# Kernel tuning notes

Hardware: AMD Instinct MI355X
Metric: run time of the kernel (lower is better)

The kernel has to match this reference:

```python
import jax, jax.numpy as jnp
import numpy as np

EPS = 1e-20
TEMP = 0.07
HEAD_DIM = 128


def setup_inputs() -> dict:
    key = jax.random.key(0)
    k1, k2, k3 = jax.random.split(key, 3)
    B, C, T, H, W = 4, 512, 8, 32, 32
    x = jax.random.normal(k1, (B, C, T, H, W), dtype=jnp.float32)
    W_head = jax.random.normal(k2, (C, HEAD_DIM), dtype=jnp.float32) / np.sqrt(C).astype(np.float32)
    b_head = jax.random.normal(k3, (HEAD_DIM,), dtype=jnp.float32) * 0.01
    return {"x": x, "W_head": W_head, "b_head": b_head}


def _forward(x, W_head, b_head):
    B, C, T, H, W = x.shape
    N = H * W
    # linear head over channel dim (equivalent to permute->Linear->permute)
    feats = jnp.einsum('bcthw,cd->bdthw', x, W_head) + b_head[None, :, None, None, None]
    keys = feats.reshape(B, HEAD_DIM, T, N)
    # F.normalize(p=2, dim=1): x / max(||x||, 1e-12)
    norm = jnp.maximum(jnp.linalg.norm(keys, axis=1, keepdims=True), 1e-12)
    keys = keys / norm
    # affinity between consecutive frames: [B, T-1, N, N]
    A = jnp.einsum('bctn,bctm->btnm', keys[:, :, :-1], keys[:, :, 1:])
    A12 = jax.nn.softmax(A / TEMP, axis=-1)                         # forward stochastic mats
    A21 = jax.nn.softmax(jnp.swapaxes(A, -1, -2) / TEMP, axis=-1)   # backward stochastic mats
    A12s = jnp.swapaxes(A12, 0, 1)  # [T-1, B, N, N]
    A21s = jnp.swapaxes(A21, 0, 1)  # [T-1, B, N, N]

    # prefix products P[i] = A12[0] @ A12[1] @ ... @ A12[i]
    def step_p(carry, a):
        c = carry @ a
        return c, c
    _, Ptail = jax.lax.scan(step_p, A12s[0], A12s[1:])
    P = jnp.concatenate([A12s[:1], Ptail], axis=0)  # [T-1, B, N, N]

    # suffix products S[i] = A21[i] @ A21[i-1] @ ... @ A21[0]
    def step_s(carry, a):
        c = a @ carry
        return c, c
    _, Stail = jax.lax.scan(step_s, A21s[0], A21s[1:])
    S = jnp.concatenate([A21s[:1], Stail], axis=0)  # [T-1, B, N, N]

    # cycle walks for i = 1..T-2: aar_i = P[i] @ S[i]
    aars = jnp.matmul(P[1:], S[1:])  # [T-2, B, N, N]
    logits = jnp.log(aars + EPS)
    # cross-entropy with identity targets: loss = logsumexp - logit[n, n]
    lse = jax.nn.logsumexp(logits, axis=-1)                  # [T-2, B, N]
    diag = jnp.diagonal(logits, axis1=-2, axis2=-1)          # [T-2, B, N]
    losses = jnp.mean(lse - diag, axis=(1, 2))               # [T-2]
    preds = jnp.argmax(logits, axis=-1)                      # [T-2, B, N]
    tgt = jnp.arange(N)[None, None, :]
    accs = jnp.mean((preds == tgt).astype(jnp.float32), axis=(1, 2))
    # original returns (loss_of_last_walk, diags); diags exposed as stacked arrays
    return losses[-1], losses, accs


def reference(x, W_head, b_head):
    return _forward(x, W_head, b_head)
```

## Files before the change

### kernel.cpp

```cpp
#include <hip/hip_runtime.h>
#include <cstdint>
#include <cstddef>

typedef unsigned short u16;
typedef unsigned long long u64;
using short8 = __attribute__((ext_vector_type(8))) short;
using f32x4  = __attribute__((ext_vector_type(4))) float;

#define KEXP 20.609929155556620f

__device__ __forceinline__ u16 f2bf(float f) {
  unsigned u = __float_as_uint(f);
  u += 0x7fffu + ((u >> 16) & 1u);
  return (u16)(u >> 16);
}
__device__ __forceinline__ float bf2f(u16 h) { return __uint_as_float(((unsigned)h) << 16); }

typedef const unsigned int GASu32 __attribute__((address_space(1)));
typedef unsigned int LASu32 __attribute__((address_space(3)));

__device__ __forceinline__ void gload16(const u16* src, u16* dstLds) {
  __builtin_amdgcn_global_load_lds((GASu32*)src, (LASu32*)dstLds, 16, 0, 0);
}

__global__ __launch_bounds__(256) void transpose_x(const float* __restrict__ x, u16* __restrict__ xT) {
  __shared__ float t[32][33];
  int b = blockIdx.z, c0 = blockIdx.y * 32, s0 = blockIdx.x * 32;
  int tid = threadIdx.x;
  int ci = tid >> 3, s4 = (tid & 7) * 4;
  float4 v = *(const float4*)(x + ((size_t)b * 512 + c0 + ci) * 8192 + s0 + s4);
  t[ci][s4 + 0] = v.x; t[ci][s4 + 1] = v.y; t[ci][s4 + 2] = v.z; t[ci][s4 + 3] = v.w;
  __syncthreads();
  int si = tid >> 3, c4 = (tid & 7) * 4;
  ushort4 o;
  o.x = f2bf(t[c4 + 0][si]); o.y = f2bf(t[c4 + 1][si]);
  o.z = f2bf(t[c4 + 2][si]); o.w = f2bf(t[c4 + 3][si]);
  *(ushort4*)(xT + ((size_t)b * 8192 + s0 + si) * 512 + c0 + c4) = o;
}

__global__ __launch_bounds__(256) void transpose_w(const float* __restrict__ W, u16* __restrict__ Wt) {
  int idx = blockIdx.x * 256 + threadIdx.x;
  int d = idx >> 9, c = idx & 511;
  Wt[idx] = f2bf(W[c * 128 + d]);
}

__global__ __launch_bounds__(256) void normalize_keys(u16* __restrict__ keys) {
  int wv = threadIdx.x >> 6, lane = threadIdx.x & 63;
  int row = blockIdx.x * 4 + wv;
  unsigned* p = (unsigned*)(keys + (size_t)row * 128) + lane;
  unsigned v = *p;
  float a = bf2f((u16)(v & 0xffffu)), b = bf2f((u16)(v >> 16));
  float s = a * a + b * b;
  #pragma unroll
  for (int m = 1; m < 64; m <<= 1) s += __shfl_xor(s, m, 64);
  float sc = 1.f / fmaxf(sqrtf(s), 1e-12f);
  *p = (unsigned)f2bf(a * sc) | ((unsigned)f2bf(b * sc) << 16);
}

__global__ __launch_bounds__(256) void k3_t0(const u16* __restrict__ E, const float* __restrict__ rsum,
                                             const float* __restrict__ csum,
                                             u16* __restrict__ P0, u16* __restrict__ S0) {
  int b = blockIdx.z, r = blockIdx.x;
  int zE = b * 7;
  const u16* e = E + ((size_t)zE << 20) + (size_t)r * 1024;
  float rr = 1.f / rsum[zE * 1024 + r];
  int c = threadIdx.x * 4;
  ushort4 v = *(const ushort4*)(e + c);
  float4 cv = *(const float4*)(csum + zE * 1024 + c);
  ushort4 o1, o2;
  float v0 = bf2f(v.x), v1 = bf2f(v.y), v2 = bf2f(v.z), v3 = bf2f(v.w);
  o1.x = f2bf(v0 * rr); o1.y = f2bf(v1 * rr); o1.z = f2bf(v2 * rr); o1.w = f2bf(v3 * rr);
  o2.x = f2bf(v0 / cv.x); o2.y = f2bf(v1 / cv.y); o2.z = f2bf(v2 / cv.z); o2.w = f2bf(v3 / cv.w);
  size_t base = ((size_t)b << 20) + (size_t)r * 1024 + c;
  *(ushort4*)(P0 + base) = o1;
  *(ushort4*)(S0 + base) = o2;
}

__global__ __launch_bounds__(256) void k3_tr(const u16* __restrict__ E, const float* __restrict__ rsum,
                                             const float* __restrict__ csum,
                                             u16* __restrict__ Bp, u16* __restrict__ Bs) {
  __shared__ u16 t[64][66];
  int z = blockIdx.z; int b = z / 6, tt = z % 6 + 1;
  int zE = b * 7 + tt;
  int er0 = blockIdx.x * 64, ec0 = blockIdx.y * 64;
  const u16* e = E + ((size_t)zE << 20);
  int tid = threadIdx.x;
  int ri = tid >> 4, c4 = (tid & 15) * 4;
  #pragma unroll
  for (int p = 0; p < 4; ++p) {
    ushort4 v = *(const ushort4*)(e + (size_t)(er0 + ri + p * 16) * 1024 + ec0 + c4);
    t[ri + p * 16][c4 + 0] = v.x; t[ri + p * 16][c4 + 1] = v.y;
    t[ri + p * 16][c4 + 2] = v.z; t[ri + p * 16][c4 + 3] = v.w;
  }
  __syncthreads();
  size_t outBase = (size_t)(b * 6 + tt - 1) << 20;
  float ir0 = 1.f / rsum[zE * 1024 + er0 + c4 + 0];
  float ir1 = 1.f / rsum[zE * 1024 + er0 + c4 + 1];
  float ir2 = 1.f / rsum[zE * 1024 + er0 + c4 + 2];
  float ir3 = 1.f / rsum[zE * 1024 + er0 + c4 + 3];
  #pragma unroll
  for (int p = 0; p < 4; ++p) {
    int roL = ri + p * 16;
    int ro = ec0 + roL;
    float ic = 1.f / csum[zE * 1024 + ro];
    float v0 = bf2f(t[c4 + 0][roL]), v1 = bf2f(t[c4 + 1][roL]);
    float v2 = bf2f(t[c4 + 2][roL]), v3 = bf2f(t[c4 + 3][roL]);
    ushort4 op, os;
    op.x = f2bf(v0 * ir0); op.y = f2bf(v1 * ir1); op.z = f2bf(v2 * ir2); op.w = f2bf(v3 * ir3);
    os.x = f2bf(v0 * ic);  os.y = f2bf(v1 * ic);  os.z = f2bf(v2 * ic);  os.w = f2bf(v3 * ic);
    size_t off = outBase + (size_t)ro * 1024 + er0 + c4;
    *(ushort4*)(Bp + off) = op;
    *(ushort4*)(Bs + off) = os;
  }
}

struct GemmBatch { const u16* A[24]; const u16* B[24]; u16* C[8]; };
enum { M_HEAD = 0, M_EXP = 1, M_PLAIN = 2, M_AAR = 3 };

__device__ __forceinline__ int lds_off32(int r, int kbyte) {
  int rp = r >> 1;
  int sl = (((r & 1) << 2) | (kbyte >> 4)) ^ (rp & 7);
  return rp * 128 + sl * 16;
}

__device__ __forceinline__ void stage_tile32(const u16* __restrict__ g, int ld, int r0, int k0, u16* lds) {
  int tid = threadIdx.x;
  #pragma unroll
  for (int j = 0; j < 2; ++j) {
    int gidx = j * 256 + tid;
    int rp = gidx >> 3, slot = gidx & 7;
    int sp = slot ^ (rp & 7);
    int r = (rp << 1) | (sp >> 2);
    int kb16 = sp & 3;
    const u16* src = g + (size_t)(r0 + r) * ld + k0 + kb16 * 8;
    gload16(src, lds + gidx * 8);
  }
}

__device__ __forceinline__ short8 frag_ld32(const u16* s, int row, int kbyte) {
  return *(const short8*)((const char*)s + lds_off32(row, kbyte));
}

#define GEMM_BODY(T, FA, FB, NA, NB)                                                    \
  {                                                                                     \
    int t_ = (T);                                                                       \
    if (t_ + 1 < nt) {                                                                  \
      if (t_ + 2 < nt) asm volatile("s_waitcnt vmcnt(4)" ::: "memory");                 \
      else             asm volatile("s_waitcnt vmcnt(0)" ::: "memory");                 \
      __builtin_amdgcn_s_barrier();                                                     \
      __builtin_amdgcn_sched_barrier(0);                                                \
      const u16* An_ = As[(t_ + 1) & 3];                                                \
      const u16* Bn_ = Bs[(t_ + 1) & 3];                                                \
      _Pragma("unroll")                                                                 \
      for (int f = 0; f < 4; ++f) {                                                     \
        NA[f] = frag_ld32(An_, (wr << 6) + (f << 4) + l15, kb);                         \
        NB[f] = frag_ld32(Bn_, (wc << 6) + (f << 4) + l15, kb);                         \
      }                                                                                 \
      if (t_ + 3 < nt) {                                                                \
        stage_tile32(A, lda, m0, (t_ + 3) << 5, As[(t_ + 3) & 3]);                      \
        stage_tile32(B, ldb, n0, (t_ + 3) << 5, Bs[(t_ + 3) & 3]);                      \
      }                                                                                 \
      asm volatile("s_waitcnt lgkmcnt(8)" ::: "memory");                                \
    } else {                                                                            \
      asm volatile("s_waitcnt lgkmcnt(0)" ::: "memory");                                \
    }                                                                                   \
    __builtin_amdgcn_sched_barrier(0);                                                  \
    __builtin_amdgcn_s_setprio(1);                                                      \
    _Pragma("unroll")                                                                   \
    for (int fr = 0; fr < 4; ++fr)                                                      \
      _Pragma("unroll")                                                                 \
      for (int fc2 = 0; fc2 < 4; ++fc2)                                                 \
        acc[fr][fc2] = __builtin_amdgcn_mfma_f32_16x16x32_bf16(FA[fr], FB[fc2],         \
                                                               acc[fr][fc2], 0, 0, 0); \
    __builtin_amdgcn_s_setprio(0);                                                      \
  }

template <int MODE>
__global__ __launch_bounds__(256) void gemm_nt(const u16* __restrict__ gA, const u16* __restrict__ gB,
                                               u16* __restrict__ gC, GemmBatch batch,
                                               const float* __restrict__ bias,
                                               float* __restrict__ rowsumR, u64* __restrict__ amax,
                                               float* __restrict__ diagv,
                                               float* __restrict__ rsumE, float* __restrict__ csumE) {
  __shared__ u16 As[4][4096];
  __shared__ u16 Bs[4][4096];
  int tid = threadIdx.x, lane = tid & 63, wv = tid >> 6;
  int wr = wv >> 1, wc = wv & 1;
  int l15 = lane & 15, kb = (lane >> 4) << 4;

  int swz;
  { int per = (int)gridDim.x >> 3; int id0 = blockIdx.x; swz = (id0 & 7) * per + (id0 >> 3); }
  int z, m0, n0;
  if constexpr (MODE == M_HEAD) { z = 0; m0 = swz << 7; n0 = 0; }
  else { z = swz >> 6; int r6 = swz & 63; m0 = (r6 & 7) << 7; n0 = (r6 >> 3) << 7; }

  const u16 *A, *B; u16* C;
  int K, lda, ldb, ldc;
  if constexpr (MODE == M_HEAD) {
    A = gA; B = gB; C = gC; K = 512; lda = 512; ldb = 512; ldc = 128;
  } else if constexpr (MODE == M_EXP) {
    int b = z / 7, t = z % 7;
    size_t offA = (size_t)(b * 8 + t) * 131072;
    A = gA + offA; B = gA + offA + 131072; C = gC + ((size_t)z << 20);
    K = 128; lda = 128; ldb = 128; ldc = 1024;
  } else if constexpr (MODE == M_PLAIN) {
    A = batch.A[z]; B = batch.B[z]; C = batch.C[z];
    K = 1024; lda = 1024; ldb = 1024; ldc = 1024;
  } else {
    A = batch.A[z]; B = batch.B[z]; C = nullptr;
    K = 1024; lda = 1024; ldb = 1024; ldc = 1024;
  }

  f32x4 acc[4][4] = {};
  int nt = K >> 5;

  stage_tile32(A, lda, m0, 0,  As[0]); stage_tile32(B, ldb, n0, 0,  Bs[0]);
  stage_tile32(A, lda, m0, 32, As[1]); stage_tile32(B, ldb, n0, 32, Bs[1]);
  stage_tile32(A, lda, m0, 64, As[2]); stage_tile32(B, ldb, n0, 64, Bs[2]);
  asm volatile("s_waitcnt vmcnt(8)" ::: "memory");
  __builtin_amdgcn_s_barrier();
  __builtin_amdgcn_sched_barrier(0);
  short8 fa0[4], fb0[4], fa1[4], fb1[4];
  #pragma unroll
  for (int f = 0; f < 4; ++f) {
    fa0[f] = frag_ld32(As[0], (wr << 6) + (f << 4) + l15, kb);
    fb0[f] = frag_ld32(Bs[0], (wc << 6) + (f << 4) + l15, kb);
  }

  for (int t = 0; t < nt; t += 2) {
    GEMM_BODY(t,     fa0, fb0, fa1, fb1);
    GEMM_BODY(t + 1, fa1, fb1, fa0, fb0);
  }

  if constexpr (MODE == M_AAR) {
    #pragma unroll
    for (int fr = 0; fr < 4; ++fr) {
      #pragma unroll
      for (int j = 0; j < 4; ++j) {
        float rs = 0.f, mv = -1.f; int mc = 0;
        #pragma unroll
        for (int fc = 0; fc < 4; ++fc) {
          float v = acc[fr][fc][j];
          rs += v;
          int c = n0 + (wc << 6) + (fc << 4) + l15;
          if (v > mv) { mv = v; mc = c; }
        }
        u64 pk = ((u64)__float_as_uint(mv) << 32) | (u64)(unsigned)(1023 - mc);
        #pragma unroll
        for (int m = 1; m < 16; m <<= 1) {
          rs += __shfl_xor(rs, m, 64);
          u64 o = __shfl_xor(pk, m, 64);
          pk = (o > pk) ? o : pk;
        }
        if (l15 == 0) {
          int row = m0 + (wr << 6) + (fr << 4) + ((lane >> 4) << 2) + j;
          atomicAdd(&rowsumR[(z << 10) + row], rs);
          atomicMax(&amax[(z << 10) + row], pk);
        }
      }
      if (m0 == n0 && wr == wc) {
        int jj = l15 - ((lane >> 4) << 2);
        if (jj >= 0 && jj < 4) {
          int row = m0 + (wr << 6) + (fr << 4) + l15;
          float dv = (jj == 0) ? acc[fr][fr][0] : (jj == 1) ? acc[fr][fr][1]
                    : (jj == 2) ? acc[fr][fr][2] : acc[fr][fr][3];
          diagv[(z << 10) + row] = dv;
        }
      }
    }
  } else if constexpr (MODE == M_EXP) {
    float rp[4][4] = {};
    float cp[4] = {};
    #pragma unroll
    for (int fr = 0; fr < 4; ++fr)
      #pragma unroll
      for (int fc = 0; fc < 4; ++fc)
        #pragma unroll
        for (int j = 0; j < 4; ++j) {
          int row = m0 + (wr << 6) + (fr << 4) + ((lane >> 4) << 2) + j;
          int col = n0 + (wc << 6) + (fc << 4) + l15;
          float v = exp2f(acc[fr][fc][j] * KEXP);
          C[(size_t)row * ldc + col] = f2bf(v);
          rp[fr][j] += v;
          cp[fc] += v;
        }
    #pragma unroll
    for (int fr = 0; fr < 4; ++fr)
      #pragma unroll
      for (int j = 0; j < 4; ++j) {
        float r = rp[fr][j];
        r += __shfl_xor(r, 1, 64); r += __shfl_xor(r, 2, 64);
        r += __shfl_xor(r, 4, 64); r += __shfl_xor(r, 8, 64);
        if (l15 == 0) {
          int row = m0 + (wr << 6) + (fr << 4) + ((lane >> 4) << 2) + j;
          atomicAdd(&rsumE[z * 1024 + row], r);
        }
      }
    #pragma unroll
    for (int fc = 0; fc < 4; ++fc) {
      float c = cp[fc];
      c += __shfl_xor(c, 16, 64); c += __shfl_xor(c, 32, 64);
      if ((lane >> 4) == 0) {
        int col = n0 + (wc << 6) + (fc << 4) + l15;
        atomicAdd(&csumE[z * 1024 + col], c);
      }
    }
  } else {
    #pragma unroll
    for (int fr = 0; fr < 4; ++fr)
      #pragma unroll
      for (int fc = 0; fc < 4; ++fc)
        #pragma unroll
        for (int j = 0; j < 4; ++j) {
          int row = m0 + (wr << 6) + (fr << 4) + ((lane >> 4) << 2) + j;
          int col = n0 + (wc << 6) + (fc << 4) + l15;
          float v = acc[fr][fc][j];
          if constexpr (MODE == M_HEAD) v += bias[col];
          C[(size_t)row * ldc + col] = f2bf(v);
        }
  }
}

__global__ __launch_bounds__(256) void finalize_k(const float* __restrict__ rowsumR, const u64* __restrict__ amax,
                                                  const float* __restrict__ diagv, float* __restrict__ out) {
  __shared__ float sl[256], sa[256];
  int w = blockIdx.x;
  int tid = threadIdx.x;
  float ls = 0.f, ac = 0.f;
  for (int idx = tid; idx < 4096; idx += 256) {
    int zi = (w << 12) + idx;
    int n = idx & 1023;
    float rs = rowsumR[zi];
    float dv = diagv[zi];
    ls += logf(rs + 1024.f * 1e-20f) - logf(dv + 1e-20f);
    unsigned pred = 1023u - (unsigned)(amax[zi] & 0xffffffffULL);
    ac += (pred == (unsigned)n) ? 1.f : 0.f;
  }
  sl[tid] = ls; sa[tid] = ac;
  __syncthreads();
  for (int s2 = 128; s2 > 0; s2 >>= 1) {
    if (tid < s2) { sl[tid] += sl[tid + s2]; sa[tid] += sa[tid + s2]; }
    __syncthreads();
  }
  if (tid == 0) {
    float loss = sl[0] / 4096.f, acv = sa[0] / 4096.f;
    out[1 + w] = loss;
    out[7 + w] = acv;
    if (w == 5) out[0] = loss;
  }
}

extern "C" void kernel_launch(void* const* d_in, const int* in_sizes, int n_in,
                              void* d_out, int out_size, void* d_ws, size_t ws_size,
                              hipStream_t stream) {
  (void)in_sizes; (void)n_in; (void)out_size; (void)ws_size;
  const float* x  = (const float*)d_in[0];
  const float* Wh = (const float*)d_in[1];
  const float* bh = (const float*)d_in[2];
  float* out = (float*)d_out;
  char* ws = (char*)d_ws;
  const size_t MB = 1ull << 20;

  u16* xT   = (u16*)(ws);
  u16* keys = (u16*)(ws + 32 * MB);
  u16* Wt   = (u16*)(ws + 40 * MB);
  float* rsumE   = (float*)(ws + 40 * MB + 128 * 1024);
  float* csumE   = (float*)(ws + 40 * MB + 240 * 1024);
  float* rowsumR = (float*)(ws + 40 * MB + 352 * 1024);
  u64*   amax    = (u64*)(ws + 40 * MB + 448 * 1024);
  float* diagv   = (float*)(ws + 40 * MB + 640 * 1024);
  u16* E    = (u16*)(ws + 41 * MB);
  u16* Bp   = (u16*)(ws + 113 * MB);
  u16* Bs   = (u16*)(ws + 161 * MB);

  u16* Pb[7] = { (u16*)(ws + 97 * MB), (u16*)(ws + 0 * MB), (u16*)(ws + 8 * MB),
                 (u16*)(ws + 16 * MB), (u16*)(ws + 24 * MB), (u16*)(ws + 41 * MB),
                 (u16*)(ws + 49 * MB) };
  u16* Sb[7] = { (u16*)(ws + 105 * MB), (u16*)(ws + 57 * MB), (u16*)(ws + 65 * MB),
                 (u16*)(ws + 73 * MB), (u16*)(ws + 81 * MB), (u16*)(ws + 89 * MB),
                 (u16*)(ws + 97 * MB) };

  GemmBatch empty{};

  transpose_x<<<dim3(256, 16, 4), 256, 0, stream>>>(x, xT);
  transpose_w<<<dim3(256), 256, 0, stream>>>(Wh, Wt);
  gemm_nt<M_HEAD><<<dim3(256), 256, 0, stream>>>(xT, Wt, keys, empty, bh,
                                                 nullptr, nullptr, nullptr, nullptr, nullptr);
  normalize_keys<<<dim3(8192), 256, 0, stream>>>(keys);
  (void)hipMemsetAsync(rsumE, 0, 512 * 1024, stream);
  gemm_nt<M_EXP><<<dim3(1792), 256, 0, stream>>>(keys, nullptr, E, empty, nullptr,
                                                 nullptr, nullptr, nullptr, rsumE, csumE);
  k3_t0<<<dim3(1024, 1, 4), 256, 0, stream>>>(E, rsumE, csumE, Pb[0], Sb[0]);
  k3_tr<<<dim3(16, 16, 24), 256, 0, stream>>>(E, rsumE, csumE, Bp, Bs);

  for (int i = 1; i <= 6; ++i) {
    GemmBatch gb{};
    for (int b = 0; b < 4; ++b) {
      gb.A[b]     = Pb[i - 1] + (size_t)b * 1048576;
      gb.B[b]     = Bp + (size_t)(b * 6 + i - 1) * 1048576;
      gb.C[b]     = Pb[i] + (size_t)b * 1048576;
      gb.A[4 + b] = Sb[i - 1] + (size_t)b * 1048576;
      gb.B[4 + b] = Bs + (size_t)(b * 6 + i - 1) * 1048576;
      gb.C[4 + b] = Sb[i] + (size_t)b * 1048576;
    }
    gemm_nt<M_PLAIN><<<dim3(512), 256, 0, stream>>>(nullptr, nullptr, nullptr, gb, nullptr,
                                                    nullptr, nullptr, nullptr, nullptr, nullptr);
  }

  GemmBatch ga{};
  for (int i = 1; i <= 6; ++i)
    for (int b = 0; b < 4; ++b) {
      ga.A[(i - 1) * 4 + b] = Pb[i] + (size_t)b * 1048576;
      ga.B[(i - 1) * 4 + b] = Sb[i] + (size_t)b * 1048576;
    }
  gemm_nt<M_AAR><<<dim3(1536), 256, 0, stream>>>(nullptr, nullptr, nullptr, ga, nullptr,
                                                 rowsumR, amax, diagv, nullptr, nullptr);
  finalize_k<<<dim3(6), 256, 0, stream>>>(rowsumR, amax, diagv, out);
}
```

Measured before the change: 314.7 us.

## Shrink GEMM LDS ring to three stages with precomputed load addresses

The GEMM pipeline's LDS ring goes from four stages to three, with rotating buffer pointers instead of modulo indexing. Per-thread global source pointers and LDS fragment offsets are now computed once before the loop rather than every iteration. Prefetch depth drops from three tiles ahead to two, and each step waits for all outstanding global loads (vmcnt(0)). This cuts address arithmetic and LDS footprint, which may allow higher occupancy, but gives less latency hiding for global loads.

```diff
diff --git a/kernel.cpp b/kernel.cpp
--- a/kernel.cpp
+++ b/kernel.cpp
@@ -123,42 +123,24 @@
   return rp * 128 + sl * 16;
 }
 
-__device__ __forceinline__ void stage_tile32(const u16* __restrict__ g, int ld, int r0, int k0, u16* lds) {
-  int tid = threadIdx.x;
-  #pragma unroll
-  for (int j = 0; j < 2; ++j) {
-    int gidx = j * 256 + tid;
-    int rp = gidx >> 3, slot = gidx & 7;
-    int sp = slot ^ (rp & 7);
-    int r = (rp << 1) | (sp >> 2);
-    int kb16 = sp & 3;
-    const u16* src = g + (size_t)(r0 + r) * ld + k0 + kb16 * 8;
-    gload16(src, lds + gidx * 8);
-  }
-}
-
-__device__ __forceinline__ short8 frag_ld32(const u16* s, int row, int kbyte) {
-  return *(const short8*)((const char*)s + lds_off32(row, kbyte));
-}
-
 #define GEMM_BODY(T, FA, FB, NA, NB)                                                    \
   {                                                                                     \
     int t_ = (T);                                                                       \
     if (t_ + 1 < nt) {                                                                  \
-      if (t_ + 2 < nt) asm volatile("s_waitcnt vmcnt(4)" ::: "memory");                 \
-      else             asm volatile("s_waitcnt vmcnt(0)" ::: "memory");                 \
+      asm volatile("s_waitcnt vmcnt(0)" ::: "memory");                                  \
       __builtin_amdgcn_s_barrier();                                                     \
       __builtin_amdgcn_sched_barrier(0);                                                \
-      const u16* An_ = As[(t_ + 1) & 3];                                                \
-      const u16* Bn_ = Bs[(t_ + 1) & 3];                                                \
       _Pragma("unroll")                                                                 \
       for (int f = 0; f < 4; ++f) {                                                     \
-        NA[f] = frag_ld32(An_, (wr << 6) + (f << 4) + l15, kb);                         \
-        NB[f] = frag_ld32(Bn_, (wc << 6) + (f << 4) + l15, kb);                         \
+        NA[f] = *(const short8*)((const char*)An + offA[f]);                            \
+        NB[f] = *(const short8*)((const char*)Bn + offB[f]);                            \
       }                                                                                 \
-      if (t_ + 3 < nt) {                                                                \
-        stage_tile32(A, lda, m0, (t_ + 3) << 5, As[(t_ + 3) & 3]);                      \
-        stage_tile32(B, ldb, n0, (t_ + 3) << 5, Bs[(t_ + 3) & 3]);                      \
+      if (t_ + 2 < nt) {                                                                \
+        int k0_ = (t_ + 2) << 5;                                                        \
+        gload16(srcA0 + k0_, At + ldso0);                                               \
+        gload16(srcA1 + k0_, At + ldso1);                                               \
+        gload16(srcB0 + k0_, Bt + ldso0);                                               \
+        gload16(srcB1 + k0_, Bt + ldso1);                                               \
       }                                                                                 \
       asm volatile("s_waitcnt lgkmcnt(8)" ::: "memory");                                \
     } else {                                                                            \
@@ -173,6 +155,8 @@
         acc[fr][fc2] = __builtin_amdgcn_mfma_f32_16x16x32_bf16(FA[fr], FB[fc2],         \
                                                                acc[fr][fc2], 0, 0, 0); \
     __builtin_amdgcn_s_setprio(0);                                                      \
+    { u16* tmpA = Ac; Ac = An; An = At; At = tmpA;                                      \
+      u16* tmpB = Bc; Bc = Bn; Bn = Bt; Bt = tmpB; }                                    \
   }
 
 template <int MODE>
@@ -182,8 +166,8 @@
                                                float* __restrict__ rowsumR, u64* __restrict__ amax,
                                                float* __restrict__ diagv,
                                                float* __restrict__ rsumE, float* __restrict__ csumE) {
-  __shared__ u16 As[4][4096];
-  __shared__ u16 Bs[4][4096];
+  __shared__ u16 AsL[3][4096];
+  __shared__ u16 BsL[3][4096];
   int tid = threadIdx.x, lane = tid & 63, wv = tid >> 6;
   int wr = wv >> 1, wc = wv & 1;
   int l15 = lane & 15, kb = (lane >> 4) << 4;
@@ -200,8 +184,8 @@
     A = gA; B = gB; C = gC; K = 512; lda = 512; ldb = 512; ldc = 128;
   } else if constexpr (MODE == M_EXP) {
     int b = z / 7, t = z % 7;
-    size_t offA = (size_t)(b * 8 + t) * 131072;
-    A = gA + offA; B = gA + offA + 131072; C = gC + ((size_t)z << 20);
+    size_t offA0 = (size_t)(b * 8 + t) * 131072;
+    A = gA + offA0; B = gA + offA0 + 131072; C = gC + ((size_t)z << 20);
     K = 128; lda = 128; ldb = 128; ldc = 1024;
   } else if constexpr (MODE == M_PLAIN) {
     A = batch.A[z]; B = batch.B[z]; C = batch.C[z];
@@ -211,20 +195,45 @@
     K = 1024; lda = 1024; ldb = 1024; ldc = 1024;
   }
 
+  const u16 *srcA0, *srcA1, *srcB0, *srcB1;
+  int ldso0, ldso1;
+  {
+    int g0 = tid, g1 = 256 + tid;
+    int rp0 = g0 >> 3, sp0 = (g0 & 7) ^ (rp0 & 7);
+    int r0_ = (rp0 << 1) | (sp0 >> 2), kb0 = (sp0 & 3) * 8;
+    int rp1 = g1 >> 3, sp1 = (g1 & 7) ^ (rp1 & 7);
+    int r1_ = (rp1 << 1) | (sp1 >> 2), kb1 = (sp1 & 3) * 8;
+    srcA0 = A + (size_t)(m0 + r0_) * lda + kb0;
+    srcA1 = A + (size_t)(m0 + r1_) * lda + kb1;
+    srcB0 = B + (size_t)(n0 + r0_) * ldb + kb0;
+    srcB1 = B + (size_t)(n0 + r1_) * ldb + kb1;
+    ldso0 = g0 * 8; ldso1 = g1 * 8;
+  }
+  int offA[4], offB[4];
+  #pragma unroll
+  for (int f = 0; f < 4; ++f) {
+    offA[f] = lds_off32((wr << 6) + (f << 4) + l15, kb);
+    offB[f] = lds_off32((wc << 6) + (f << 4) + l15, kb);
+  }
+
   f32x4 acc[4][4] = {};
   int nt = K >> 5;
 
-  stage_tile32(A, lda, m0, 0,  As[0]); stage_tile32(B, ldb, n0, 0,  Bs[0]);
-  stage_tile32(A, lda, m0, 32, As[1]); stage_tile32(B, ldb, n0, 32, Bs[1]);
-  stage_tile32(A, lda, m0, 64, As[2]); stage_tile32(B, ldb, n0, 64, Bs[2]);
-  asm volatile("s_waitcnt vmcnt(8)" ::: "memory");
+  u16 *Ac = AsL[0], *An = AsL[1], *At = AsL[2];
+  u16 *Bc = BsL[0], *Bn = BsL[1], *Bt = BsL[2];
+
+  gload16(srcA0 +  0, Ac + ldso0); gload16(srcA1 +  0, Ac + ldso1);
+  gload16(srcB0 +  0, Bc + ldso0); gload16(srcB1 +  0, Bc + ldso1);
+  gload16(srcA0 + 32, An + ldso0); gload16(srcA1 + 32, An + ldso1);
+  gload16(srcB0 + 32, Bn + ldso0); gload16(srcB1 + 32, Bn + ldso1);
+  asm volatile("s_waitcnt vmcnt(4)" ::: "memory");
   __builtin_amdgcn_s_barrier();
   __builtin_amdgcn_sched_barrier(0);
   short8 fa0[4], fb0[4], fa1[4], fb1[4];
   #pragma unroll
   for (int f = 0; f < 4; ++f) {
-    fa0[f] = frag_ld32(As[0], (wr << 6) + (f << 4) + l15, kb);
-    fb0[f] = frag_ld32(Bs[0], (wc << 6) + (f << 4) + l15, kb);
+    fa0[f] = *(const short8*)((const char*)Ac + offA[f]);
+    fb0[f] = *(const short8*)((const char*)Bc + offB[f]);
   }
 
   for (int t = 0; t < nt; t += 2) {
```

New measurement: 324.9 us. 1.03x slower.

## Fuse cycle-walk AAR GEMMs into chain GEMM launches and drop atomics

Applied to the files above, without the earlier changes.

The separate batched AAR GEMM launch is removed. Each walk's P[i]@S[i] GEMM now runs inside the same launch as the next chain step, so the chain launches, which only fill 512 blocks, get extra independent blocks. Per-row sums and argmax are written as per-column-block partials instead of global atomics, and the finalize kernel reduces the 16 partials. This removes a memset, the atomic traffic and one large launch. In exchange it adds extra partial-buffer traffic, and the chain kernel carries a branchy epilogue.

```diff
diff --git a/kernel.cpp b/kernel.cpp
--- a/kernel.cpp
+++ b/kernel.cpp
@@ -115,7 +115,7 @@
 }
 
 struct GemmBatch { const u16* A[24]; const u16* B[24]; u16* C[8]; };
-enum { M_HEAD = 0, M_EXP = 1, M_PLAIN = 2, M_AAR = 3 };
+enum { M_HEAD = 0, M_EXP = 1 };
 
 __device__ __forceinline__ int lds_off32(int r, int kbyte) {
   int rp = r >> 1;
@@ -177,10 +177,8 @@
 
 template <int MODE>
 __global__ __launch_bounds__(256) void gemm_nt(const u16* __restrict__ gA, const u16* __restrict__ gB,
-                                               u16* __restrict__ gC, GemmBatch batch,
+                                               u16* __restrict__ gC,
                                                const float* __restrict__ bias,
-                                               float* __restrict__ rowsumR, u64* __restrict__ amax,
-                                               float* __restrict__ diagv,
                                                float* __restrict__ rsumE, float* __restrict__ csumE) {
   __shared__ u16 As[4][4096];
   __shared__ u16 Bs[4][4096];
@@ -198,17 +196,11 @@
   int K, lda, ldb, ldc;
   if constexpr (MODE == M_HEAD) {
     A = gA; B = gB; C = gC; K = 512; lda = 512; ldb = 512; ldc = 128;
-  } else if constexpr (MODE == M_EXP) {
+  } else {
     int b = z / 7, t = z % 7;
-    size_t offA = (size_t)(b * 8 + t) * 131072;
-    A = gA + offA; B = gA + offA + 131072; C = gC + ((size_t)z << 20);
+    size_t offA0 = (size_t)(b * 8 + t) * 131072;
+    A = gA + offA0; B = gA + offA0 + 131072; C = gC + ((size_t)z << 20);
     K = 128; lda = 128; ldb = 128; ldc = 1024;
-  } else if constexpr (MODE == M_PLAIN) {
-    A = batch.A[z]; B = batch.B[z]; C = batch.C[z];
-    K = 1024; lda = 1024; ldb = 1024; ldc = 1024;
-  } else {
-    A = batch.A[z]; B = batch.B[z]; C = nullptr;
-    K = 1024; lda = 1024; ldb = 1024; ldc = 1024;
   }
 
   f32x4 acc[4][4] = {};
@@ -226,49 +218,12 @@
     fa0[f] = frag_ld32(As[0], (wr << 6) + (f << 4) + l15, kb);
     fb0[f] = frag_ld32(Bs[0], (wc << 6) + (f << 4) + l15, kb);
   }
-
   for (int t = 0; t < nt; t += 2) {
     GEMM_BODY(t,     fa0, fb0, fa1, fb1);
     GEMM_BODY(t + 1, fa1, fb1, fa0, fb0);
   }
 
-  if constexpr (MODE == M_AAR) {
-    #pragma unroll
-    for (int fr = 0; fr < 4; ++fr) {
-      #pragma unroll
-      for (int j = 0; j < 4; ++j) {
-        float rs = 0.f, mv = -1.f; int mc = 0;
-        #pragma unroll
-        for (int fc = 0; fc < 4; ++fc) {
-          float v = acc[fr][fc][j];
-          rs += v;
-          int c = n0 + (wc << 6) + (fc << 4) + l15;
-          if (v > mv) { mv = v; mc = c; }
-        }
-        u64 pk = ((u64)__float_as_uint(mv) << 32) | (u64)(unsigned)(1023 - mc);
-        #pragma unroll
-        for (int m = 1; m < 16; m <<= 1) {
-          rs += __shfl_xor(rs, m, 64);
-          u64 o = __shfl_xor(pk, m, 64);
-          pk = (o > pk) ? o : pk;
-        }
-        if (l15 == 0) {
-          int row = m0 + (wr << 6) + (fr << 4) + ((lane >> 4) << 2) + j;
-          atomicAdd(&rowsumR[(z << 10) + row], rs);
-          atomicMax(&amax[(z << 10) + row], pk);
-        }
-      }
-      if (m0 == n0 && wr == wc) {
-        int jj = l15 - ((lane >> 4) << 2);
-        if (jj >= 0 && jj < 4) {
-          int row = m0 + (wr << 6) + (fr << 4) + l15;
-          float dv = (jj == 0) ? acc[fr][fr][0] : (jj == 1) ? acc[fr][fr][1]
-                    : (jj == 2) ? acc[fr][fr][2] : acc[fr][fr][3];
-          diagv[(z << 10) + row] = dv;
-        }
-      }
-    }
-  } else if constexpr (MODE == M_EXP) {
+  if constexpr (MODE == M_EXP) {
     float rp[4][4] = {};
     float cp[4] = {};
     #pragma unroll
@@ -314,26 +269,123 @@
         for (int j = 0; j < 4; ++j) {
           int row = m0 + (wr << 6) + (fr << 4) + ((lane >> 4) << 2) + j;
           int col = n0 + (wc << 6) + (fc << 4) + l15;
+          C[(size_t)row * ldc + col] = f2bf(acc[fr][fc][j] + bias[col]);
+        }
+  }
+}
+
+__global__ __launch_bounds__(256) void gemm_ca(GemmBatch gb, int nChain,
+                                               float* __restrict__ rsPw, u64* __restrict__ amPw,
+                                               float* __restrict__ diagw) {
+  __shared__ u16 As[4][4096];
+  __shared__ u16 Bs[4][4096];
+  int tid = threadIdx.x, lane = tid & 63, wv = tid >> 6;
+  int wr = wv >> 1, wc = wv & 1;
+  int l15 = lane & 15, kb = (lane >> 4) << 4;
+
+  int swz;
+  { int per = (int)gridDim.x >> 3; int id0 = blockIdx.x; swz = (id0 & 7) * per + (id0 >> 3); }
+  bool isChain = swz < nChain;
+  int work = isChain ? swz : swz - nChain;
+  int zr = work >> 6, r6 = work & 63;
+  int m0 = (r6 & 7) << 7, n0 = (r6 >> 3) << 7;
+  const u16* A = isChain ? gb.A[zr] : gb.A[8 + zr];
+  const u16* B = isChain ? gb.B[zr] : gb.B[8 + zr];
+  const int lda = 1024, ldb = 1024;
+  const int nt = 32;
+
+  f32x4 acc[4][4] = {};
+
+  stage_tile32(A, lda, m0, 0,  As[0]); stage_tile32(B, ldb, n0, 0,  Bs[0]);
+  stage_tile32(A, lda, m0, 32, As[1]); stage_tile32(B, ldb, n0, 32, Bs[1]);
+  stage_tile32(A, lda, m0, 64, As[2]); stage_tile32(B, ldb, n0, 64, Bs[2]);
+  asm volatile("s_waitcnt vmcnt(8)" ::: "memory");
+  __builtin_amdgcn_s_barrier();
+  __builtin_amdgcn_sched_barrier(0);
+  short8 fa0[4], fb0[4], fa1[4], fb1[4];
+  #pragma unroll
+  for (int f = 0; f < 4; ++f) {
+    fa0[f] = frag_ld32(As[0], (wr << 6) + (f << 4) + l15, kb);
+    fb0[f] = frag_ld32(Bs[0], (wc << 6) + (f << 4) + l15, kb);
+  }
+  for (int t = 0; t < nt; t += 2) {
+    GEMM_BODY(t,     fa0, fb0, fa1, fb1);
+    GEMM_BODY(t + 1, fa1, fb1, fa0, fb0);
+  }
+
+  if (isChain) {
+    u16* C = gb.C[zr];
+    #pragma unroll
+    for (int fr = 0; fr < 4; ++fr)
+      #pragma unroll
+      for (int fc = 0; fc < 4; ++fc)
+        #pragma unroll
+        for (int j = 0; j < 4; ++j) {
+          int row = m0 + (wr << 6) + (fr << 4) + ((lane >> 4) << 2) + j;
+          int col = n0 + (wc << 6) + (fc << 4) + l15;
+          C[(size_t)row * 1024 + col] = f2bf(acc[fr][fc][j]);
+        }
+  } else {
+    int nb = n0 >> 7;
+    size_t pbase = (size_t)zr * 16384 + (size_t)((nb << 1) | wc) * 1024;
+    #pragma unroll
+    for (int fr = 0; fr < 4; ++fr) {
+      #pragma unroll
+      for (int j = 0; j < 4; ++j) {
+        float rs = 0.f, mv = -1.f; int mc = 0;
+        #pragma unroll
+        for (int fc = 0; fc < 4; ++fc) {
           float v = acc[fr][fc][j];
-          if constexpr (MODE == M_HEAD) v += bias[col];
-          C[(size_t)row * ldc + col] = f2bf(v);
-        }
-  }
-}
-
-__global__ __launch_bounds__(256) void finalize_k(const float* __restrict__ rowsumR, const u64* __restrict__ amax,
+          rs += v;
+          int c = n0 + (wc << 6) + (fc << 4) + l15;
+          if (v > mv) { mv = v; mc = c; }
+        }
+        u64 pk = ((u64)__float_as_uint(mv) << 32) | (u64)(unsigned)(1023 - mc);
+        #pragma unroll
+        for (int m = 1; m < 16; m <<= 1) {
+          rs += __shfl_xor(rs, m, 64);
+          u64 o = __shfl_xor(pk, m, 64);
+          pk = (o > pk) ? o : pk;
+        }
+        if (l15 == 0) {
+          int row = m0 + (wr << 6) + (fr << 4) + ((lane >> 4) << 2) + j;
+          rsPw[pbase + row] = rs;
+          amPw[pbase + row] = pk;
+        }
+      }
+      if (m0 == n0 && wr == wc) {
+        int jj = l15 - ((lane >> 4) << 2);
+        if (jj >= 0 && jj < 4) {
+          int row = m0 + (wr << 6) + (fr << 4) + l15;
+          float dv = (jj == 0) ? acc[fr][fr][0] : (jj == 1) ? acc[fr][fr][1]
+                    : (jj == 2) ? acc[fr][fr][2] : acc[fr][fr][3];
+          diagw[(zr << 10) + row] = dv;
+        }
+      }
+    }
+  }
+}
+
+__global__ __launch_bounds__(256) void finalize_k(const float* __restrict__ rsP, const u64* __restrict__ amP,
                                                   const float* __restrict__ diagv, float* __restrict__ out) {
   __shared__ float sl[256], sa[256];
   int w = blockIdx.x;
   int tid = threadIdx.x;
   float ls = 0.f, ac = 0.f;
   for (int idx = tid; idx < 4096; idx += 256) {
-    int zi = (w << 12) + idx;
-    int n = idx & 1023;
-    float rs = rowsumR[zi];
-    float dv = diagv[zi];
+    int b = idx >> 10, n = idx & 1023;
+    int z = (w << 2) + b;
+    size_t base = (size_t)z * 16384 + n;
+    float rs = 0.f; u64 pk = 0;
+    #pragma unroll
+    for (int k = 0; k < 16; ++k) {
+      rs += rsP[base + k * 1024];
+      u64 o = amP[base + k * 1024];
+      pk = (o > pk) ? o : pk;
+    }
+    float dv = diagv[(z << 10) + n];
     ls += logf(rs + 1024.f * 1e-20f) - logf(dv + 1e-20f);
-    unsigned pred = 1023u - (unsigned)(amax[zi] & 0xffffffffULL);
+    unsigned pred = 1023u - (unsigned)(pk & 0xffffffffULL);
     ac += (pred == (unsigned)n) ? 1.f : 0.f;
   }
   sl[tid] = ls; sa[tid] = ac;
@@ -363,12 +415,12 @@
 
   u16* xT   = (u16*)(ws);
   u16* keys = (u16*)(ws + 32 * MB);
+  float* rsP   = (float*)(ws + 32 * MB);
+  u64*   amP   = (u64*)(ws + 34 * MB);
+  float* diagv = (float*)(ws + 38 * MB);
   u16* Wt   = (u16*)(ws + 40 * MB);
-  float* rsumE   = (float*)(ws + 40 * MB + 128 * 1024);
-  float* csumE   = (float*)(ws + 40 * MB + 240 * 1024);
-  float* rowsumR = (float*)(ws + 40 * MB + 352 * 1024);
-  u64*   amax    = (u64*)(ws + 40 * MB + 448 * 1024);
-  float* diagv   = (float*)(ws + 40 * MB + 640 * 1024);
+  float* rsumE = (float*)(ws + 40 * MB + 128 * 1024);
+  float* csumE = (float*)(ws + 40 * MB + 240 * 1024);
   u16* E    = (u16*)(ws + 41 * MB);
   u16* Bp   = (u16*)(ws + 113 * MB);
   u16* Bs   = (u16*)(ws + 161 * MB);
@@ -380,16 +432,12 @@
                  (u16*)(ws + 73 * MB), (u16*)(ws + 81 * MB), (u16*)(ws + 89 * MB),
                  (u16*)(ws + 97 * MB) };
 
-  GemmBatch empty{};
-
   transpose_x<<<dim3(256, 16, 4), 256, 0, stream>>>(x, xT);
   transpose_w<<<dim3(256), 256, 0, stream>>>(Wh, Wt);
-  gemm_nt<M_HEAD><<<dim3(256), 256, 0, stream>>>(xT, Wt, keys, empty, bh,
-                                                 nullptr, nullptr, nullptr, nullptr, nullptr);
+  gemm_nt<M_HEAD><<<dim3(256), 256, 0, stream>>>(xT, Wt, keys, bh, nullptr, nullptr);
   normalize_keys<<<dim3(8192), 256, 0, stream>>>(keys);
-  (void)hipMemsetAsync(rsumE, 0, 512 * 1024, stream);
-  gemm_nt<M_EXP><<<dim3(1792), 256, 0, stream>>>(keys, nullptr, E, empty, nullptr,
-                                                 nullptr, nullptr, nullptr, rsumE, csumE);
+  (void)hipMemsetAsync(rsumE, 0, 224 * 1024, stream);
+  gemm_nt<M_EXP><<<dim3(1792), 256, 0, stream>>>(keys, nullptr, E, nullptr, rsumE, csumE);
   k3_t0<<<dim3(1024, 1, 4), 256, 0, stream>>>(E, rsumE, csumE, Pb[0], Sb[0]);
   k3_tr<<<dim3(16, 16, 24), 256, 0, stream>>>(E, rsumE, csumE, Bp, Bs);
 
@@ -403,17 +451,31 @@
       gb.B[4 + b] = Bs + (size_t)(b * 6 + i - 1) * 1048576;
       gb.C[4 + b] = Sb[i] + (size_t)b * 1048576;
     }
-    gemm_nt<M_PLAIN><<<dim3(512), 256, 0, stream>>>(nullptr, nullptr, nullptr, gb, nullptr,
-                                                    nullptr, nullptr, nullptr, nullptr, nullptr);
-  }
-
-  GemmBatch ga{};
-  for (int i = 1; i <= 6; ++i)
+    int grid = 512;
+    float* rsPw = nullptr; u64* amPw = nullptr; float* dgw = nullptr;
+    if (i >= 2) {
+      grid = 768;
+      int w = i - 1;
+      for (int b = 0; b < 4; ++b) {
+        gb.A[8 + b] = Pb[w] + (size_t)b * 1048576;
+        gb.B[8 + b] = Sb[w] + (size_t)b * 1048576;
+      }
+      rsPw = rsP + (size_t)(w - 1) * 65536;
+      amPw = amP + (size_t)(w - 1) * 65536;
+      dgw  = diagv + (size_t)(w - 1) * 4096;
+    }
+    gemm_ca<<<dim3(grid), 256, 0, stream>>>(gb, 512, rsPw, amPw, dgw);
+  }
+  {
+    GemmBatch gb{};
     for (int b = 0; b < 4; ++b) {
-      ga.A[(i - 1) * 4 + b] = Pb[i] + (size_t)b * 1048576;
-      ga.B[(i - 1) * 4 + b] = Sb[i] + (size_t)b * 1048576;
-    }
-  gemm_nt<M_AAR><<<dim3(1536), 256, 0, stream>>>(nullptr, nullptr, nullptr, ga, nullptr,
-                                                 rowsumR, amax, diagv, nullptr, nullptr);
-  finalize_k<<<dim3(6), 256, 0, stream>>>(rowsumR, amax, diagv, out);
-}
+      gb.A[8 + b] = Pb[6] + (size_t)b * 1048576;
+      gb.B[8 + b] = Sb[6] + (size_t)b * 1048576;
+    }
+    gemm_ca<<<dim3(256), 256, 0, stream>>>(gb, 0,
+                                           rsP + (size_t)5 * 65536,
+                                           amP + (size_t)5 * 65536,
+                                           diagv + (size_t)5 * 4096);
+  }
+  finalize_k<<<dim3(6), 256, 0, stream>>>(rsP, amP, diagv, out);
+}
```

Result: slower. 372.8 us (+18.5%).
